# Performance work log

Measured on AMD Instinct MI355X. Metric: run time of the kernel, lower is better.

The kernel has to match this reference:

```python
import jax, jax.numpy as jnp
import numpy as np

D_MODEL = 1024
HEADDIM = 64
EXPAND = 2
D_STATE = 128
D_CONV = 4
NGROUPS = 1
D_INNER = EXPAND * D_MODEL            # 2048
NHEADS = D_INNER // HEADDIM           # 32
CONV_DIM = D_INNER + 2 * NGROUPS * D_STATE
D_IN_PROJ = 2 * D_INNER + 2 * NGROUPS * D_STATE + NHEADS
BATCH = 2
SEQLEN = 1024
EPS = 1e-5


def silu(v):
    return v * jax.nn.sigmoid(v)


def setup_inputs() -> dict:
    key = jax.random.key(0)
    ks = jax.random.split(key, 8)
    s = 0.02
    return {
        "x": jax.random.normal(ks[0], (BATCH, SEQLEN, D_MODEL), jnp.float32),
        "in_proj_w": jax.random.normal(ks[1], (D_IN_PROJ, D_MODEL), jnp.float32) * s,
        "conv_w": jax.random.normal(ks[2], (CONV_DIM, D_CONV), jnp.float32) * 0.2,
        "conv_b": jax.random.normal(ks[3], (CONV_DIM,), jnp.float32) * 0.02,
        "dt_bias": jax.random.normal(ks[4], (NHEADS,), jnp.float32) * 0.1,
        "A_log": jax.random.normal(ks[5], (NHEADS,), jnp.float32) * 0.5,
        "D": jax.random.normal(ks[6], (NHEADS,), jnp.float32) * 0.5,
        "norm_w": jnp.ones((D_INNER,), jnp.float32),
        "out_proj_w": jax.random.normal(ks[7], (D_MODEL, D_INNER), jnp.float32) * s,
    }


def _mamba2(x, in_proj_w, conv_w, conv_b, dt_bias, A_log, D, norm_w, out_proj_w):
    b, l, _ = x.shape
    # input projection -> z | xBC | dt
    zxbcdt = x @ in_proj_w.T                                  # [b,l,d_in_proj]
    z, xBC, dt = jnp.split(zxbcdt, [D_INNER, D_INNER + CONV_DIM], axis=-1)
    dt = jax.nn.softplus(dt + dt_bias)                        # [b,l,nh]
    # causal depthwise conv over time, then SiLU
    rhs = conv_w.T[:, None, :]                                # [d_conv, 1, conv_dim]
    xBC = jax.lax.conv_general_dilated(
        xBC, rhs, window_strides=(1,), padding=[(D_CONV - 1, 0)],
        dimension_numbers=("NWC", "WIO", "NWC"), feature_group_count=CONV_DIM)
    xBC = silu(xBC + conv_b)
    xs, Bm, Cm = jnp.split(xBC, [D_INNER, D_INNER + D_STATE], axis=-1)
    xs = xs.reshape(b, l, NHEADS, HEADDIM)                    # [b,l,h,p]
    A = -jnp.exp(A_log)                                       # [nh], negative
    dA = jnp.exp(dt * A)                                      # [b,l,nh] in (0,1)
    # selective scan: h_t = dA_t * h_{t-1} + dt_t * x_t (outer) B_t; y_t = h_t C_t
    def step(h, inp):
        dA_t, x_t, B_t, dt_t, C_t = inp                       # [b,h],[b,h,p],[b,n],[b,h],[b,n]
        h = h * dA_t[:, :, None, None] + jnp.einsum("bh,bhp,bn->bhpn", dt_t, x_t, B_t)
        y = jnp.einsum("bhpn,bn->bhp", h, C_t)
        return h, y

    h0 = jnp.zeros((b, NHEADS, HEADDIM, D_STATE), x.dtype)
    xs_t = xs.transpose(1, 0, 2, 3)
    _, ys = jax.lax.scan(step, h0, (dA.transpose(1, 0, 2), xs_t,
                                    Bm.transpose(1, 0, 2), dt.transpose(1, 0, 2),
                                    Cm.transpose(1, 0, 2)))
    y = ys.transpose(1, 0, 2, 3) + D[None, None, :, None] * xs  # skip term
    y = y.reshape(b, l, D_INNER)
    # gated RMSNorm (norm_before_gate=False): rmsnorm(y * silu(z)) * w
    y = y * silu(z)
    y = y * jax.lax.rsqrt(jnp.mean(y * y, axis=-1, keepdims=True) + EPS) * norm_w
    return y @ out_proj_w.T


def reference(x, in_proj_w, conv_w, conv_b, dt_bias, A_log, D, norm_w, out_proj_w):
    return x + _mamba2(x, in_proj_w, conv_w, conv_b, dt_bias, A_log, D, norm_w, out_proj_w)
```

## Files before the change

kernel.cpp:

```cpp
#include <hip/hip_runtime.h>
#include <hip/hip_bf16.h>
#include <math.h>

#define NHEADS   32
#define CONV_DIM 2304
#define D_INNER  2048
#define SEQLEN   1024
#define NROWS    2048
#define ZX_STR   4352
#define D_MODEL  1024
#define Q        64
#define NCHUNK   16
#define XT_STR   72

typedef __attribute__((ext_vector_type(8))) short bhalf8;
typedef __attribute__((ext_vector_type(8))) short short8;
typedef __attribute__((ext_vector_type(4))) short short4v;
typedef __attribute__((ext_vector_type(4))) float f32x4;

__device__ __forceinline__ float bf2f(__hip_bfloat16 v){ return __bfloat162float(v); }
__device__ __forceinline__ short f2bs(float f){ __hip_bfloat16 h = __float2bfloat16(f); return *(short*)&h; }
__device__ __forceinline__ float s2f(short s){ __hip_bfloat16 h = *(__hip_bfloat16*)&s; return __bfloat162float(h); }
__device__ __forceinline__ float rdin(const void* p, size_t i, int isf){
    return isf ? ((const float*)p)[i] : __bfloat162float(((const __hip_bfloat16*)p)[i]);
}

__global__ __launch_bounds__(256)
void detect_dtype(const unsigned short* __restrict__ p, int* __restrict__ flag,
                  float* __restrict__ rowsum)
{
    for (int i = threadIdx.x; i < NROWS; i += 256) rowsum[i] = 0.f;
    int cnt = 0;
    for (int i = threadIdx.x; i < 4096; i += 256) {
        unsigned short u = p[2 * i];
        int e = (u >> 7) & 0xFF;
        cnt += (e >= 90 && e <= 141) ? 1 : 0;
    }
#pragma unroll
    for (int m = 1; m < 64; m <<= 1) cnt += __shfl_xor(cnt, m);
    __shared__ int red[4];
    if ((threadIdx.x & 63) == 0) red[threadIdx.x >> 6] = cnt;
    __syncthreads();
    if (threadIdx.x == 0) *flag = ((red[0]+red[1]+red[2]+red[3]) < 2048) ? 1 : 0;
}

#define XN8 262144
#define WN8 561152
#define ON8 262144
__global__ __launch_bounds__(256)
void to_bf16_all(const void* __restrict__ xs, const void* __restrict__ ws,
                 const void* __restrict__ os, const void* __restrict__ normw,
                 __hip_bfloat16* __restrict__ xd, __hip_bfloat16* __restrict__ wd,
                 __hip_bfloat16* __restrict__ od, const int* __restrict__ flagp)
{
    const int isf = *flagp;
    int i = blockIdx.x * 256 + threadIdx.x;
    if (i < XN8 + WN8) {
        const void* src; __hip_bfloat16* dst; int j;
        if (i < XN8) { src = xs; dst = xd; j = i; }
        else         { src = ws; dst = wd; j = i - XN8; }
        if (isf) {
            const float4* s = (const float4*)src;
            float4 a = s[2 * j], b = s[2 * j + 1];
            short8 r;
            r[0]=f2bs(a.x); r[1]=f2bs(a.y); r[2]=f2bs(a.z); r[3]=f2bs(a.w);
            r[4]=f2bs(b.x); r[5]=f2bs(b.y); r[6]=f2bs(b.z); r[7]=f2bs(b.w);
            ((short8*)dst)[j] = r;
        } else {
            ((float4*)dst)[j] = ((const float4*)src)[j];
        }
    } else {
        int j = i - XN8 - WN8;
        int k0 = (j * 8) & (D_INNER - 1);
        float v[8];
        if (isf) {
            const float4* s = (const float4*)os;
            float4 a = s[2 * j], b = s[2 * j + 1];
            v[0]=a.x; v[1]=a.y; v[2]=a.z; v[3]=a.w;
            v[4]=b.x; v[5]=b.y; v[6]=b.z; v[7]=b.w;
        } else {
            bhalf8 a = ((const bhalf8*)os)[j];
#pragma unroll
            for (int q = 0; q < 8; ++q) v[q] = s2f(a[q]);
        }
        short8 r;
#pragma unroll
        for (int q = 0; q < 8; ++q)
            r[q] = f2bs(v[q] * rdin(normw, k0 + q, isf));
        ((short8*)od)[j] = r;
    }
}

template<int MODE, int MT, int NT, int WROWS, int WCOLS>
__global__ __launch_bounds__(256)
void gemm_bt(const __hip_bfloat16* __restrict__ A,
             const __hip_bfloat16* __restrict__ W,
             __hip_bfloat16* __restrict__ Cb,
             const void* __restrict__ xraw,
             void* __restrict__ outv,
             const float* __restrict__ rowsum,
             const int* __restrict__ flagp,
             int K, int N)
{
    constexpr int FM = MT / WROWS / 16;
    constexpr int FN = NT / WCOLS / 16;
    constexpr int AI = MT / 32;
    constexpr int BI = NT / 32;
    __shared__ short As[MT * 64];
    __shared__ short Bs[NT * 64];
    const int m0 = blockIdx.y * MT;
    const int n0 = blockIdx.x * NT;
    const int wave = threadIdx.x >> 6;
    const int lane = threadIdx.x & 63;
    const int lr8 = lane >> 3, lc8 = lane & 7;
    const int lr  = lane & 15, lq  = lane >> 4;
    const int wm = (wave / WCOLS) * (MT / WROWS);
    const int wn = (wave % WCOLS) * (NT / WCOLS);
    const int swl = lr & 7;

    f32x4 acc[FM][FN];
#pragma unroll
    for (int i = 0; i < FM; ++i)
#pragma unroll
        for (int j = 0; j < FN; ++j) acc[i][j] = (f32x4){0.f,0.f,0.f,0.f};

    for (int k0 = 0; k0 < K; k0 += 64) {
#pragma unroll
        for (int i = 0; i < AI; ++i) {
            const int rt = (wave * AI + i) * 8;
            const __hip_bfloat16* gp = A + (size_t)(m0 + rt + lr8) * K + k0 + ((lc8 ^ lr8) << 3);
            __builtin_amdgcn_global_load_lds(
                (const __attribute__((address_space(1))) void*)gp,
                (__attribute__((address_space(3))) void*)&As[rt * 64], 16, 0, 0);
        }
#pragma unroll
        for (int i = 0; i < BI; ++i) {
            const int rt = (wave * BI + i) * 8;
            const __hip_bfloat16* gp = W + (size_t)(n0 + rt + lr8) * K + k0 + ((lc8 ^ lr8) << 3);
            __builtin_amdgcn_global_load_lds(
                (const __attribute__((address_space(1))) void*)gp,
                (__attribute__((address_space(3))) void*)&Bs[rt * 64], 16, 0, 0);
        }
        __syncthreads();
#pragma unroll
        for (int kk = 0; kk < 64; kk += 32) {
            const int sw = (((kk >> 3) + lq) ^ swl) << 3;
            bhalf8 af[FM], bfv[FN];
#pragma unroll
            for (int t = 0; t < FM; ++t)
                af[t]  = *(const bhalf8*)&As[(wm + t * 16 + lr) * 64 + sw];
#pragma unroll
            for (int t = 0; t < FN; ++t)
                bfv[t] = *(const bhalf8*)&Bs[(wn + t * 16 + lr) * 64 + sw];
#pragma unroll
            for (int ti = 0; ti < FM; ++ti)
#pragma unroll
                for (int tj = 0; tj < FN; ++tj)
                    acc[ti][tj] = __builtin_amdgcn_mfma_f32_16x16x32_bf16(
                        af[ti], bfv[tj], acc[ti][tj], 0, 0, 0);
        }
        __syncthreads();
    }

    const int isf = (MODE == 1) ? *flagp : 0;
#pragma unroll
    for (int ti = 0; ti < FM; ++ti)
#pragma unroll
        for (int tj = 0; tj < FN; ++tj)
#pragma unroll
            for (int r = 0; r < 4; ++r) {
                int m = m0 + wm + ti * 16 + lq * 4 + r;
                int n = n0 + wn + tj * 16 + lr;
                size_t idx = (size_t)m * N + n;
                float v = acc[ti][tj][r];
                if (MODE == 0) {
                    Cb[idx] = __float2bfloat16(v);
                } else {
                    float scale = rsqrtf(rowsum[m] / (float)D_INNER + 1e-5f);
                    v = v * scale + rdin(xraw, idx, isf);
                    if (isf) ((float*)outv)[idx] = v;
                    else     ((__hip_bfloat16*)outv)[idx] = __float2bfloat16(v);
                }
            }
}

__global__ __launch_bounds__(256)
void convdt(const __hip_bfloat16* __restrict__ zxb,
            const void* __restrict__ conv_w, const void* __restrict__ conv_b,
            const void* __restrict__ xraw, const void* __restrict__ wraw,
            const void* __restrict__ dt_bias,
            const int* __restrict__ flagp,
            __hip_bfloat16* __restrict__ xs_bf,
            __hip_bfloat16* __restrict__ B_bf,
            __hip_bfloat16* __restrict__ C_bf,
            float* __restrict__ dtp)
{
    __shared__ short smem[11 * CONV_DIM];
    const int isf = *flagp;

    if (blockIdx.x < 256) {
        const int r0 = blockIdx.x * 8;
        const int bstart = r0 & ~(SEQLEN - 1);
        for (int idx = threadIdx.x; idx < 11 * (CONV_DIM / 8); idx += 256) {
            int ii = idx / (CONV_DIM / 8);
            int seg = idx % (CONV_DIM / 8);
            int g = r0 - 3 + ii;
            bhalf8 v;
            if (g >= bstart) {
                v = *(const bhalf8*)&zxb[(size_t)g * ZX_STR + 2048 + seg * 8];
            } else {
#pragma unroll
                for (int j = 0; j < 8; ++j) v[j] = 0;
            }
            *(bhalf8*)&smem[ii * CONV_DIM + seg * 8] = v;
        }
        __syncthreads();

#pragma unroll
        for (int sIt = 0; sIt < 2; ++sIt) {
            const int seg = threadIdx.x + sIt * 256;
            if (seg >= CONV_DIM / 8) break;
            const int c0 = seg * 8;
            float wt[8][4], bias[8];
            if (isf) {
                const float4* wp = (const float4*)conv_w;
#pragma unroll
                for (int u = 0; u < 8; ++u) {
                    float4 q = wp[c0 + u];
                    wt[u][0]=q.x; wt[u][1]=q.y; wt[u][2]=q.z; wt[u][3]=q.w;
                }
                float4 b0 = ((const float4*)conv_b)[seg * 2];
                float4 b1 = ((const float4*)conv_b)[seg * 2 + 1];
                bias[0]=b0.x; bias[1]=b0.y; bias[2]=b0.z; bias[3]=b0.w;
                bias[4]=b1.x; bias[5]=b1.y; bias[6]=b1.z; bias[7]=b1.w;
            } else {
                const bhalf8* wp = (const bhalf8*)conv_w;
#pragma unroll
                for (int u = 0; u < 4; ++u) {
                    bhalf8 q = wp[seg * 4 + u];
#pragma unroll
                    for (int t4 = 0; t4 < 4; ++t4) {
                        wt[2*u][t4]   = s2f(q[t4]);
                        wt[2*u+1][t4] = s2f(q[4 + t4]);
                    }
                }
                bhalf8 bq = ((const bhalf8*)conv_b)[seg];
#pragma unroll
                for (int j = 0; j < 8; ++j) bias[j] = s2f(bq[j]);
            }
#pragma unroll
            for (int r = 0; r < 8; ++r) {
                bhalf8 i0 = *(const bhalf8*)&smem[(r + 0) * CONV_DIM + c0];
                bhalf8 i1 = *(const bhalf8*)&smem[(r + 1) * CONV_DIM + c0];
                bhalf8 i2 = *(const bhalf8*)&smem[(r + 2) * CONV_DIM + c0];
                bhalf8 i3 = *(const bhalf8*)&smem[(r + 3) * CONV_DIM + c0];
                bhalf8 out;
#pragma unroll
                for (int j = 0; j < 8; ++j) {
                    float acc = bias[j];
                    acc = fmaf(s2f(i0[j]), wt[j][0], acc);
                    acc = fmaf(s2f(i1[j]), wt[j][1], acc);
                    acc = fmaf(s2f(i2[j]), wt[j][2], acc);
                    acc = fmaf(s2f(i3[j]), wt[j][3], acc);
                    out[j] = f2bs(acc / (1.f + expf(-acc)));
                }
                const int row = r0 + r;
                if (c0 < 2048)
                    *(bhalf8*)&xs_bf[(size_t)row * 2048 + c0] = out;
                else if (c0 < 2176)
                    *(bhalf8*)&B_bf[(size_t)row * 128 + (c0 - 2048)] = out;
                else
                    *(bhalf8*)&C_bf[(size_t)row * 128 + (c0 - 2176)] = out;
            }
        }
    } else {
        float* xsh = (float*)smem;
        const int r0 = (blockIdx.x - 256) * 8;
        if (isf) {
            const float4* xp = (const float4*)xraw;
            for (int i4 = threadIdx.x; i4 < 2048; i4 += 256)
                *(float4*)&xsh[i4 * 4] = xp[(size_t)r0 * 256 + i4];
        } else {
            const bhalf8* xp = (const bhalf8*)xraw;
            for (int i8 = threadIdx.x; i8 < 1024; i8 += 256) {
                bhalf8 v = xp[(size_t)r0 * 128 + i8];
#pragma unroll
                for (int q = 0; q < 8; ++q) xsh[i8 * 8 + q] = s2f(v[q]);
            }
        }
        __syncthreads();
        const int h = threadIdx.x >> 3;
        const int t = threadIdx.x & 7;
        const size_t wb = (size_t)(4352 + h) * D_MODEL;
        float s[8];
#pragma unroll
        for (int r = 0; r < 8; ++r) s[r] = 0.f;
        if (isf) {
            const float4* wp = (const float4*)wraw;
            for (int k0 = 0; k0 < D_MODEL; k0 += 32) {
                float4 w4 = wp[(wb + k0) / 4 + t];
#pragma unroll
                for (int r = 0; r < 8; ++r) {
                    float4 x4 = *(const float4*)&xsh[r * D_MODEL + k0 + t * 4];
                    s[r] = fmaf(w4.x, x4.x, fmaf(w4.y, x4.y,
                           fmaf(w4.z, x4.z, fmaf(w4.w, x4.w, s[r]))));
                }
            }
        } else {
            const __hip_bfloat16* wp = (const __hip_bfloat16*)wraw;
            for (int k0 = 0; k0 < D_MODEL; k0 += 64) {
                bhalf8 w8 = *(const bhalf8*)&wp[wb + k0 + t * 8];
#pragma unroll
                for (int r = 0; r < 8; ++r) {
                    float4 xa = *(const float4*)&xsh[r * D_MODEL + k0 + t * 8];
                    float4 xb = *(const float4*)&xsh[r * D_MODEL + k0 + t * 8 + 4];
                    s[r] = fmaf(s2f(w8[0]), xa.x, fmaf(s2f(w8[1]), xa.y,
                           fmaf(s2f(w8[2]), xa.z, fmaf(s2f(w8[3]), xa.w, s[r]))));
                    s[r] = fmaf(s2f(w8[4]), xb.x, fmaf(s2f(w8[5]), xb.y,
                           fmaf(s2f(w8[6]), xb.z, fmaf(s2f(w8[7]), xb.w, s[r]))));
                }
            }
        }
#pragma unroll
        for (int r = 0; r < 8; ++r) {
            s[r] += __shfl_xor(s[r], 1);
            s[r] += __shfl_xor(s[r], 2);
            s[r] += __shfl_xor(s[r], 4);
        }
        if (t == 0) {
            float bias = rdin(dt_bias, h, isf);
#pragma unroll
            for (int r = 0; r < 8; ++r) {
                float raw = s[r] + bias;
                dtp[(size_t)(r0 + r) * NHEADS + h] = raw > 20.f ? raw : log1pf(expf(raw));
            }
        }
    }
}

__global__ __launch_bounds__(256)
void chunk_kernel(const __hip_bfloat16* __restrict__ xs_bf,
                  const __hip_bfloat16* __restrict__ B_bf,
                  const __hip_bfloat16* __restrict__ C_bf,
                  const float* __restrict__ dtp, const void* __restrict__ Alog,
                  const int* __restrict__ flagp,
                  float* __restrict__ cumg, float* __restrict__ decayg,
                  __hip_bfloat16* __restrict__ M_bf,
                  __hip_bfloat16* __restrict__ Sb)
{
    __shared__ float cumS[Q], uS[Q], dtS[Q];
    __shared__ short Xt[64 * XT_STR];
    __shared__ short Bt[128 * XT_STR];
    const int bhc = blockIdx.x;
    const int c = bhc & 15, h = (bhc >> 4) & 31, b = bhc >> 9;
    const int row0 = b * SEQLEN + c * Q;
    const int isf = *flagp;

    if (threadIdx.x < 64) {
        const int t = threadIdx.x;
        const float An = -expf(rdin(Alog, h, isf));
        const float dt = dtp[(size_t)(row0 + t) * NHEADS + h];
        float cum = dt * An;
#pragma unroll
        for (int ofs = 1; ofs < 64; ofs <<= 1) {
            float v = __shfl_up(cum, ofs);
            if (t >= ofs) cum += v;
        }
        float tot = __shfl(cum, 63);
        cumS[t] = cum; dtS[t] = dt;
        uS[t] = expf(tot - cum) * dt;
        cumg[(size_t)bhc * Q + t] = cum;
        if (t == 63) decayg[bhc] = expf(tot);
    }
    __syncthreads();

#pragma unroll
    for (int i = 0; i < 2; ++i) {
        int seg = threadIdx.x + i * 256;
        int t = seg >> 3, p8 = (seg & 7) * 8;
        float ut = uS[t];
        bhalf8 v = *(const bhalf8*)&xs_bf[(size_t)(row0 + t) * 2048 + h * 64 + p8];
#pragma unroll
        for (int j = 0; j < 8; ++j)
            Xt[(p8 + j) * XT_STR + t] = f2bs(s2f(v[j]) * ut);
    }
#pragma unroll
    for (int i = 0; i < 4; ++i) {
        int seg = threadIdx.x + i * 256;
        int t = seg >> 4, n8 = (seg & 15) * 8;
        bhalf8 v = *(const bhalf8*)&B_bf[(size_t)(row0 + t) * 128 + n8];
#pragma unroll
        for (int j = 0; j < 8; ++j)
            Bt[(n8 + j) * XT_STR + t] = v[j];
    }

    const int wave = threadIdx.x >> 6, lane = threadIdx.x & 63;
    const int lr = lane & 15, lq = lane >> 4;

    {
        const int t0 = wave * 16;
        f32x4 acc[4];
#pragma unroll
        for (int j = 0; j < 4; ++j) acc[j] = (f32x4){0.f,0.f,0.f,0.f};
#pragma unroll
        for (int kk = 0; kk < 128; kk += 32) {
            bhalf8 af = *(const bhalf8*)&C_bf[(size_t)(row0 + t0 + lr) * 128 + kk + lq * 8];
#pragma unroll
            for (int j = 0; j < 4; ++j) {
                bhalf8 bf = *(const bhalf8*)&B_bf[(size_t)(row0 + j * 16 + lr) * 128 + kk + lq * 8];
                acc[j] = __builtin_amdgcn_mfma_f32_16x16x32_bf16(af, bf, acc[j], 0, 0, 0);
            }
        }
#pragma unroll
        for (int j = 0; j < 4; ++j)
#pragma unroll
            for (int r = 0; r < 4; ++r) {
                int t = t0 + lq * 4 + r;
                int s = j * 16 + lr;
                float m = (s <= t) ? acc[j][r] * expf(cumS[t] - cumS[s]) * dtS[s] : 0.f;
                M_bf[(size_t)bhc * 4096 + t * 64 + s] = __float2bfloat16(m);
            }
    }
    __syncthreads();

    {
        const int p0 = wave * 16;
        f32x4 acc[8];
#pragma unroll
        for (int j = 0; j < 8; ++j) acc[j] = (f32x4){0.f,0.f,0.f,0.f};
#pragma unroll
        for (int kk = 0; kk < 64; kk += 32) {
            bhalf8 af = *(const bhalf8*)&Xt[(p0 + lr) * XT_STR + kk + lq * 8];
#pragma unroll
            for (int j = 0; j < 8; ++j) {
                bhalf8 bf = *(const bhalf8*)&Bt[(j * 16 + lr) * XT_STR + kk + lq * 8];
                acc[j] = __builtin_amdgcn_mfma_f32_16x16x32_bf16(af, bf, acc[j], 0, 0, 0);
            }
        }
#pragma unroll
        for (int j = 0; j < 8; ++j)
#pragma unroll
            for (int r = 0; r < 4; ++r) {
                int p = p0 + lq * 4 + r;
                int n = j * 16 + lr;
                Sb[(size_t)bhc * 8192 + p * 128 + n] = __float2bfloat16(acc[j][r]);
            }
    }
}

__global__ __launch_bounds__(256)
void rec_kernel(const __hip_bfloat16* __restrict__ Sb,
                const float* __restrict__ decayg,
                __hip_bfloat16* __restrict__ hst)
{
    const int bh = blockIdx.x >> 3;
    const int sl = blockIdx.x & 7;
    const int off = sl * 1024 + threadIdx.x * 4;
    float h0 = 0.f, h1 = 0.f, h2 = 0.f, h3 = 0.f;
    for (int c = 0; c < NCHUNK; ++c) {
        size_t base = ((size_t)bh * NCHUNK + c) * 8192 + off;
        short4v hb;
        hb[0] = f2bs(h0); hb[1] = f2bs(h1); hb[2] = f2bs(h2); hb[3] = f2bs(h3);
        *(short4v*)&hst[base] = hb;
        short4v sv = *(const short4v*)&Sb[base];
        float d = decayg[bh * NCHUNK + c];
        h0 = fmaf(h0, d, s2f(sv[0])); h1 = fmaf(h1, d, s2f(sv[1]));
        h2 = fmaf(h2, d, s2f(sv[2])); h3 = fmaf(h3, d, s2f(sv[3]));
    }
}

__global__ __launch_bounds__(256)
void y_kernel(const __hip_bfloat16* __restrict__ M_bf,
              const __hip_bfloat16* __restrict__ xs_bf,
              const __hip_bfloat16* __restrict__ C_bf,
              const __hip_bfloat16* __restrict__ hst,
              const float* __restrict__ cumg,
              const __hip_bfloat16* __restrict__ zxb,
              const void* __restrict__ Draw, const int* __restrict__ flagp,
              __hip_bfloat16* __restrict__ vbuf, float* __restrict__ rowsum)
{
    __shared__ short Xt[64 * XT_STR];
    __shared__ short zS[64 * XT_STR];
    const int bhc = blockIdx.x;
    const int c = bhc & 15, h = (bhc >> 4) & 31, b = bhc >> 9;
    const int row0 = b * SEQLEN + c * Q;
    const int isf = *flagp;
    const float Dh = rdin(Draw, h, isf);

#pragma unroll
    for (int i = 0; i < 2; ++i) {
        int seg = threadIdx.x + i * 256;
        int t = seg >> 3, p8 = (seg & 7) * 8;
        bhalf8 v = *(const bhalf8*)&xs_bf[(size_t)(row0 + t) * 2048 + h * 64 + p8];
#pragma unroll
        for (int j = 0; j < 8; ++j)
            Xt[(p8 + j) * XT_STR + t] = v[j];
        bhalf8 zv = *(const bhalf8*)&zxb[(size_t)(row0 + t) * ZX_STR + h * 64 + p8];
        *(bhalf8*)&zS[t * XT_STR + p8] = zv;
    }
    __syncthreads();

    const int wave = threadIdx.x >> 6, lane = threadIdx.x & 63;
    const int lr = lane & 15, lq = lane >> 4;
    const int t0 = wave * 16;
    f32x4 acc1[4], acc2[4];
#pragma unroll
    for (int j = 0; j < 4; ++j) { acc1[j] = (f32x4){0.f,0.f,0.f,0.f}; acc2[j] = acc1[j]; }

#pragma unroll
    for (int kk = 0; kk < 64; kk += 32) {
        bhalf8 af = *(const bhalf8*)&M_bf[(size_t)bhc * 4096 + (t0 + lr) * 64 + kk + lq * 8];
#pragma unroll
        for (int j = 0; j < 4; ++j) {
            bhalf8 bf = *(const bhalf8*)&Xt[(j * 16 + lr) * XT_STR + kk + lq * 8];
            acc1[j] = __builtin_amdgcn_mfma_f32_16x16x32_bf16(af, bf, acc1[j], 0, 0, 0);
        }
    }
#pragma unroll
    for (int kk = 0; kk < 128; kk += 32) {
        bhalf8 af = *(const bhalf8*)&C_bf[(size_t)(row0 + t0 + lr) * 128 + kk + lq * 8];
#pragma unroll
        for (int j = 0; j < 4; ++j) {
            bhalf8 bf = *(const bhalf8*)&hst[(size_t)bhc * 8192 + (j * 16 + lr) * 128 + kk + lq * 8];
            acc2[j] = __builtin_amdgcn_mfma_f32_16x16x32_bf16(af, bf, acc2[j], 0, 0, 0);
        }
    }
    float ex[4];
#pragma unroll
    for (int r = 0; r < 4; ++r) ex[r] = expf(cumg[(size_t)bhc * Q + t0 + lq * 4 + r]);

    float vv[4][4];
    float s2[4] = {0.f, 0.f, 0.f, 0.f};
#pragma unroll
    for (int j = 0; j < 4; ++j)
#pragma unroll
        for (int r = 0; r < 4; ++r) {
            int t = t0 + lq * 4 + r;
            int p = j * 16 + lr;
            float xv = s2f(Xt[p * XT_STR + t]);
            float y = acc1[j][r] + ex[r] * acc2[j][r] + Dh * xv;
            float zz = s2f(zS[t * XT_STR + p]);
            float v = y * (zz / (1.f + expf(-zz)));
            vv[j][r] = v;
            s2[r] += v * v;
        }
#pragma unroll
    for (int r = 0; r < 4; ++r) {
        s2[r] += __shfl_xor(s2[r], 1);
        s2[r] += __shfl_xor(s2[r], 2);
        s2[r] += __shfl_xor(s2[r], 4);
        s2[r] += __shfl_xor(s2[r], 8);
    }
    if (lr == 0)
#pragma unroll
        for (int r = 0; r < 4; ++r)
            atomicAdd(&rowsum[row0 + t0 + lq * 4 + r], s2[r]);

    __syncthreads();
#pragma unroll
    for (int j = 0; j < 4; ++j)
#pragma unroll
        for (int r = 0; r < 4; ++r)
            zS[(t0 + lq * 4 + r) * XT_STR + j * 16 + lr] = f2bs(vv[j][r]);
    __syncthreads();
#pragma unroll
    for (int i = 0; i < 2; ++i) {
        int seg = threadIdx.x + i * 256;
        int t = seg >> 3, p8 = (seg & 7) * 8;
        bhalf8 o = *(const bhalf8*)&zS[t * XT_STR + p8];
        *(bhalf8*)&vbuf[(size_t)(row0 + t) * D_INNER + h * 64 + p8] = o;
    }
}

extern "C" void kernel_launch(void* const* d_in, const int* in_sizes, int n_in,
                              void* d_out, int out_size, void* d_ws, size_t ws_size,
                              hipStream_t stream)
{
    const void* x_raw    = d_in[0];
    const void* inw_raw  = d_in[1];
    const void* convw    = d_in[2];
    const void* convb    = d_in[3];
    const void* dtb      = d_in[4];
    const void* Alog     = d_in[5];
    const void* Dsk      = d_in[6];
    const void* normw    = d_in[7];
    const void* outw_raw = d_in[8];

    char* ws = (char*)d_ws;
    size_t off = 0;
    int* flag = (int*)(ws + off);                      off += 256;
    float* rowsum = (float*)(ws + off);                off += (size_t)NROWS * 4;
    __hip_bfloat16* xb    = (__hip_bfloat16*)(ws+off); off += (size_t)NROWS * D_MODEL * 2;
    __hip_bfloat16* inwb  = (__hip_bfloat16*)(ws+off); off += (size_t)4384 * D_MODEL * 2;
    __hip_bfloat16* outwb = (__hip_bfloat16*)(ws+off); off += (size_t)D_MODEL * D_INNER * 2;
    __hip_bfloat16* zxb   = (__hip_bfloat16*)(ws+off); off += (size_t)NROWS * ZX_STR * 2;
    __hip_bfloat16* xs_bf = (__hip_bfloat16*)(ws+off); off += (size_t)NROWS * 2048 * 2;
    __hip_bfloat16* B_bf  = (__hip_bfloat16*)(ws+off); off += (size_t)NROWS * 128 * 2;
    __hip_bfloat16* C_bf  = (__hip_bfloat16*)(ws+off); off += (size_t)NROWS * 128 * 2;
    float* dtp   = (float*)(ws+off);                   off += (size_t)NROWS * NHEADS * 4;
    float* cumg  = (float*)(ws+off);                   off += (size_t)1024 * Q * 4;
    float* decayg= (float*)(ws+off);                   off += (size_t)1024 * 4;
    __hip_bfloat16* M_bf  = (__hip_bfloat16*)(ws+off); off += (size_t)1024 * 4096 * 2;
    __hip_bfloat16* hst   = (__hip_bfloat16*)(ws+off); off += (size_t)1024 * 8192 * 2;
    __hip_bfloat16* Sb    = (__hip_bfloat16*)(ws+off); off += (size_t)1024 * 8192 * 2;
    __hip_bfloat16* vbuf = Sb;

    detect_dtype<<<1, 256, 0, stream>>>((const unsigned short*)x_raw, flag, rowsum);
    to_bf16_all<<<(XN8+WN8+ON8)/256, 256, 0, stream>>>(x_raw, inw_raw, outw_raw,
                                                       normw, xb, inwb, outwb, flag);
    gemm_bt<0,64,128,1,4><<<dim3(34, 32), 256, 0, stream>>>(
        xb, inwb, zxb, nullptr, nullptr, nullptr, flag, D_MODEL, ZX_STR);
    convdt<<<512, 256, 0, stream>>>(zxb, convw, convb, x_raw, inw_raw, dtb, flag,
                                    xs_bf, B_bf, C_bf, dtp);
    chunk_kernel<<<1024, 256, 0, stream>>>(xs_bf, B_bf, C_bf, dtp, Alog, flag,
                                           cumg, decayg, M_bf, Sb);
    rec_kernel<<<512, 256, 0, stream>>>(Sb, decayg, hst);
    y_kernel<<<1024, 256, 0, stream>>>(M_bf, xs_bf, C_bf, hst, cumg, zxb, Dsk,
                                       flag, vbuf, rowsum);
    gemm_bt<1,64,64,2,2><<<dim3(16, 32), 256, 0, stream>>>(
        vbuf, outwb, nullptr, x_raw, d_out, rowsum, flag, D_INNER, D_MODEL);
}
```

Measured before the change: 224.6 us.

## Compute intra-chunk CB mask matrix in y_kernel and fold dtype detection into conversion

The C·B^T masked decay matrix M is now computed inside y_kernel and kept in shared memory, so it no longer has to be written to global memory by chunk_kernel and read back. Dtype detection moves into every block of the bf16 conversion kernel, which removes one tiny serial launch. The rowsum zeroing moves to chunk_kernel. In exchange, each conversion block redundantly reads 4096 samples to recompute the flag, and y_kernel uses more shared memory and does more work.

```diff
diff --git a/kernel.cpp b/kernel.cpp
--- a/kernel.cpp
+++ b/kernel.cpp
@@ -25,25 +25,6 @@
     return isf ? ((const float*)p)[i] : __bfloat162float(((const __hip_bfloat16*)p)[i]);
 }
 
-__global__ __launch_bounds__(256)
-void detect_dtype(const unsigned short* __restrict__ p, int* __restrict__ flag,
-                  float* __restrict__ rowsum)
-{
-    for (int i = threadIdx.x; i < NROWS; i += 256) rowsum[i] = 0.f;
-    int cnt = 0;
-    for (int i = threadIdx.x; i < 4096; i += 256) {
-        unsigned short u = p[2 * i];
-        int e = (u >> 7) & 0xFF;
-        cnt += (e >= 90 && e <= 141) ? 1 : 0;
-    }
-#pragma unroll
-    for (int m = 1; m < 64; m <<= 1) cnt += __shfl_xor(cnt, m);
-    __shared__ int red[4];
-    if ((threadIdx.x & 63) == 0) red[threadIdx.x >> 6] = cnt;
-    __syncthreads();
-    if (threadIdx.x == 0) *flag = ((red[0]+red[1]+red[2]+red[3]) < 2048) ? 1 : 0;
-}
-
 #define XN8 262144
 #define WN8 561152
 #define ON8 262144
@@ -51,9 +32,22 @@
 void to_bf16_all(const void* __restrict__ xs, const void* __restrict__ ws,
                  const void* __restrict__ os, const void* __restrict__ normw,
                  __hip_bfloat16* __restrict__ xd, __hip_bfloat16* __restrict__ wd,
-                 __hip_bfloat16* __restrict__ od, const int* __restrict__ flagp)
+                 __hip_bfloat16* __restrict__ od, int* __restrict__ flagp)
 {
-    const int isf = *flagp;
+    const unsigned short* xu = (const unsigned short*)xs;
+    int cnt = 0;
+    for (int k = threadIdx.x; k < 4096; k += 256) {
+        int e = (xu[2 * k] >> 7) & 0xFF;
+        cnt += (e >= 90 && e <= 141) ? 1 : 0;
+    }
+#pragma unroll
+    for (int m = 1; m < 64; m <<= 1) cnt += __shfl_xor(cnt, m);
+    __shared__ int red[4];
+    if ((threadIdx.x & 63) == 0) red[threadIdx.x >> 6] = cnt;
+    __syncthreads();
+    const int isf = ((red[0] + red[1] + red[2] + red[3]) < 2048) ? 1 : 0;
+    if (blockIdx.x == 0 && threadIdx.x == 0) *flagp = isf;
+
     int i = blockIdx.x * 256 + threadIdx.x;
     if (i < XN8 + WN8) {
         const void* src; __hip_bfloat16* dst; int j;
@@ -341,14 +335,13 @@
 __global__ __launch_bounds__(256)
 void chunk_kernel(const __hip_bfloat16* __restrict__ xs_bf,
                   const __hip_bfloat16* __restrict__ B_bf,
-                  const __hip_bfloat16* __restrict__ C_bf,
                   const float* __restrict__ dtp, const void* __restrict__ Alog,
                   const int* __restrict__ flagp,
                   float* __restrict__ cumg, float* __restrict__ decayg,
-                  __hip_bfloat16* __restrict__ M_bf,
-                  __hip_bfloat16* __restrict__ Sb)
+                  __hip_bfloat16* __restrict__ Sb,
+                  float* __restrict__ rowsum)
 {
-    __shared__ float cumS[Q], uS[Q], dtS[Q];
+    __shared__ float cumS[Q], uS[Q];
     __shared__ short Xt[64 * XT_STR];
     __shared__ short Bt[128 * XT_STR];
     const int bhc = blockIdx.x;
@@ -356,6 +349,7 @@
     const int row0 = b * SEQLEN + c * Q;
     const int isf = *flagp;
 
+    if (threadIdx.x < 2) rowsum[bhc * 2 + threadIdx.x] = 0.f;
     if (threadIdx.x < 64) {
         const int t = threadIdx.x;
         const float An = -expf(rdin(Alog, h, isf));
@@ -367,7 +361,7 @@
             if (t >= ofs) cum += v;
         }
         float tot = __shfl(cum, 63);
-        cumS[t] = cum; dtS[t] = dt;
+        cumS[t] = cum;
         uS[t] = expf(tot - cum) * dt;
         cumg[(size_t)bhc * Q + t] = cum;
         if (t == 63) decayg[bhc] = expf(tot);
@@ -393,59 +387,31 @@
         for (int j = 0; j < 8; ++j)
             Bt[(n8 + j) * XT_STR + t] = v[j];
     }
+    __syncthreads();
 
     const int wave = threadIdx.x >> 6, lane = threadIdx.x & 63;
     const int lr = lane & 15, lq = lane >> 4;
-
-    {
-        const int t0 = wave * 16;
-        f32x4 acc[4];
-#pragma unroll
-        for (int j = 0; j < 4; ++j) acc[j] = (f32x4){0.f,0.f,0.f,0.f};
-#pragma unroll
-        for (int kk = 0; kk < 128; kk += 32) {
-            bhalf8 af = *(const bhalf8*)&C_bf[(size_t)(row0 + t0 + lr) * 128 + kk + lq * 8];
-#pragma unroll
-            for (int j = 0; j < 4; ++j) {
-                bhalf8 bf = *(const bhalf8*)&B_bf[(size_t)(row0 + j * 16 + lr) * 128 + kk + lq * 8];
-                acc[j] = __builtin_amdgcn_mfma_f32_16x16x32_bf16(af, bf, acc[j], 0, 0, 0);
-            }
-        }
-#pragma unroll
-        for (int j = 0; j < 4; ++j)
-#pragma unroll
-            for (int r = 0; r < 4; ++r) {
-                int t = t0 + lq * 4 + r;
-                int s = j * 16 + lr;
-                float m = (s <= t) ? acc[j][r] * expf(cumS[t] - cumS[s]) * dtS[s] : 0.f;
-                M_bf[(size_t)bhc * 4096 + t * 64 + s] = __float2bfloat16(m);
-            }
-    }
-    __syncthreads();
-
-    {
-        const int p0 = wave * 16;
-        f32x4 acc[8];
-#pragma unroll
-        for (int j = 0; j < 8; ++j) acc[j] = (f32x4){0.f,0.f,0.f,0.f};
-#pragma unroll
-        for (int kk = 0; kk < 64; kk += 32) {
-            bhalf8 af = *(const bhalf8*)&Xt[(p0 + lr) * XT_STR + kk + lq * 8];
-#pragma unroll
-            for (int j = 0; j < 8; ++j) {
-                bhalf8 bf = *(const bhalf8*)&Bt[(j * 16 + lr) * XT_STR + kk + lq * 8];
-                acc[j] = __builtin_amdgcn_mfma_f32_16x16x32_bf16(af, bf, acc[j], 0, 0, 0);
-            }
-        }
-#pragma unroll
-        for (int j = 0; j < 8; ++j)
-#pragma unroll
-            for (int r = 0; r < 4; ++r) {
-                int p = p0 + lq * 4 + r;
-                int n = j * 16 + lr;
-                Sb[(size_t)bhc * 8192 + p * 128 + n] = __float2bfloat16(acc[j][r]);
-            }
-    }
+    const int p0 = wave * 16;
+    f32x4 acc[8];
+#pragma unroll
+    for (int j = 0; j < 8; ++j) acc[j] = (f32x4){0.f,0.f,0.f,0.f};
+#pragma unroll
+    for (int kk = 0; kk < 64; kk += 32) {
+        bhalf8 af = *(const bhalf8*)&Xt[(p0 + lr) * XT_STR + kk + lq * 8];
+#pragma unroll
+        for (int j = 0; j < 8; ++j) {
+            bhalf8 bf = *(const bhalf8*)&Bt[(j * 16 + lr) * XT_STR + kk + lq * 8];
+            acc[j] = __builtin_amdgcn_mfma_f32_16x16x32_bf16(af, bf, acc[j], 0, 0, 0);
+        }
+    }
+#pragma unroll
+    for (int j = 0; j < 8; ++j)
+#pragma unroll
+        for (int r = 0; r < 4; ++r) {
+            int p = p0 + lq * 4 + r;
+            int n = j * 16 + lr;
+            Sb[(size_t)bhc * 8192 + p * 128 + n] = __float2bfloat16(acc[j][r]);
+        }
 }
 
 __global__ __launch_bounds__(256)
@@ -470,23 +436,30 @@
 }
 
 __global__ __launch_bounds__(256)
-void y_kernel(const __hip_bfloat16* __restrict__ M_bf,
-              const __hip_bfloat16* __restrict__ xs_bf,
+void y_kernel(const __hip_bfloat16* __restrict__ xs_bf,
+              const __hip_bfloat16* __restrict__ B_bf,
               const __hip_bfloat16* __restrict__ C_bf,
               const __hip_bfloat16* __restrict__ hst,
               const float* __restrict__ cumg,
+              const float* __restrict__ dtp,
               const __hip_bfloat16* __restrict__ zxb,
               const void* __restrict__ Draw, const int* __restrict__ flagp,
               __hip_bfloat16* __restrict__ vbuf, float* __restrict__ rowsum)
 {
     __shared__ short Xt[64 * XT_STR];
     __shared__ short zS[64 * XT_STR];
+    __shared__ short Mt[64 * XT_STR];
+    __shared__ float cumS[Q], dtS[Q];
     const int bhc = blockIdx.x;
     const int c = bhc & 15, h = (bhc >> 4) & 31, b = bhc >> 9;
     const int row0 = b * SEQLEN + c * Q;
     const int isf = *flagp;
     const float Dh = rdin(Draw, h, isf);
 
+    if (threadIdx.x < 64) {
+        cumS[threadIdx.x] = cumg[(size_t)bhc * Q + threadIdx.x];
+        dtS[threadIdx.x]  = dtp[(size_t)(row0 + threadIdx.x) * NHEADS + h];
+    }
 #pragma unroll
     for (int i = 0; i < 2; ++i) {
         int seg = threadIdx.x + i * 256;
@@ -503,13 +476,38 @@
     const int wave = threadIdx.x >> 6, lane = threadIdx.x & 63;
     const int lr = lane & 15, lq = lane >> 4;
     const int t0 = wave * 16;
+
+    {
+        f32x4 accg[4];
+#pragma unroll
+        for (int j = 0; j < 4; ++j) accg[j] = (f32x4){0.f,0.f,0.f,0.f};
+#pragma unroll
+        for (int kk = 0; kk < 128; kk += 32) {
+            bhalf8 af = *(const bhalf8*)&C_bf[(size_t)(row0 + t0 + lr) * 128 + kk + lq * 8];
+#pragma unroll
+            for (int j = 0; j < 4; ++j) {
+                bhalf8 bf = *(const bhalf8*)&B_bf[(size_t)(row0 + j * 16 + lr) * 128 + kk + lq * 8];
+                accg[j] = __builtin_amdgcn_mfma_f32_16x16x32_bf16(af, bf, accg[j], 0, 0, 0);
+            }
+        }
+#pragma unroll
+        for (int j = 0; j < 4; ++j)
+#pragma unroll
+            for (int r = 0; r < 4; ++r) {
+                int t = t0 + lq * 4 + r;
+                int s = j * 16 + lr;
+                float m = (s <= t) ? accg[j][r] * expf(cumS[t] - cumS[s]) * dtS[s] : 0.f;
+                Mt[t * XT_STR + s] = f2bs(m);
+            }
+    }
+    __syncthreads();
+
     f32x4 acc1[4], acc2[4];
 #pragma unroll
     for (int j = 0; j < 4; ++j) { acc1[j] = (f32x4){0.f,0.f,0.f,0.f}; acc2[j] = acc1[j]; }
-
 #pragma unroll
     for (int kk = 0; kk < 64; kk += 32) {
-        bhalf8 af = *(const bhalf8*)&M_bf[(size_t)bhc * 4096 + (t0 + lr) * 64 + kk + lq * 8];
+        bhalf8 af = *(const bhalf8*)&Mt[(t0 + lr) * XT_STR + kk + lq * 8];
 #pragma unroll
         for (int j = 0; j < 4; ++j) {
             bhalf8 bf = *(const bhalf8*)&Xt[(j * 16 + lr) * XT_STR + kk + lq * 8];
@@ -527,7 +525,7 @@
     }
     float ex[4];
 #pragma unroll
-    for (int r = 0; r < 4; ++r) ex[r] = expf(cumg[(size_t)bhc * Q + t0 + lq * 4 + r]);
+    for (int r = 0; r < 4; ++r) ex[r] = expf(cumS[t0 + lq * 4 + r]);
 
     float vv[4][4];
     float s2[4] = {0.f, 0.f, 0.f, 0.f};
@@ -600,23 +598,21 @@
     float* dtp   = (float*)(ws+off);                   off += (size_t)NROWS * NHEADS * 4;
     float* cumg  = (float*)(ws+off);                   off += (size_t)1024 * Q * 4;
     float* decayg= (float*)(ws+off);                   off += (size_t)1024 * 4;
-    __hip_bfloat16* M_bf  = (__hip_bfloat16*)(ws+off); off += (size_t)1024 * 4096 * 2;
     __hip_bfloat16* hst   = (__hip_bfloat16*)(ws+off); off += (size_t)1024 * 8192 * 2;
     __hip_bfloat16* Sb    = (__hip_bfloat16*)(ws+off); off += (size_t)1024 * 8192 * 2;
     __hip_bfloat16* vbuf = Sb;
 
-    detect_dtype<<<1, 256, 0, stream>>>((const unsigned short*)x_raw, flag, rowsum);
     to_bf16_all<<<(XN8+WN8+ON8)/256, 256, 0, stream>>>(x_raw, inw_raw, outw_raw,
                                                        normw, xb, inwb, outwb, flag);
     gemm_bt<0,64,128,1,4><<<dim3(34, 32), 256, 0, stream>>>(
         xb, inwb, zxb, nullptr, nullptr, nullptr, flag, D_MODEL, ZX_STR);
     convdt<<<512, 256, 0, stream>>>(zxb, convw, convb, x_raw, inw_raw, dtb, flag,
                                     xs_bf, B_bf, C_bf, dtp);
-    chunk_kernel<<<1024, 256, 0, stream>>>(xs_bf, B_bf, C_bf, dtp, Alog, flag,
-                                           cumg, decayg, M_bf, Sb);
+    chunk_kernel<<<1024, 256, 0, stream>>>(xs_bf, B_bf, dtp, Alog, flag,
+                                           cumg, decayg, Sb, rowsum);
     rec_kernel<<<512, 256, 0, stream>>>(Sb, decayg, hst);
-    y_kernel<<<1024, 256, 0, stream>>>(M_bf, xs_bf, C_bf, hst, cumg, zxb, Dsk,
-                                       flag, vbuf, rowsum);
+    y_kernel<<<1024, 256, 0, stream>>>(xs_bf, B_bf, C_bf, hst, cumg, dtp, zxb,
+                                       Dsk, flag, vbuf, rowsum);
     gemm_bt<1,64,64,2,2><<<dim3(16, 32), 256, 0, stream>>>(
         vbuf, outwb, nullptr, x_raw, d_out, rowsum, flag, D_INNER, D_MODEL);
 }
```

New measurement: 225.2 us. No clear change (+0.3%).
